# Performance work log

Measured on AMD Instinct MI355X. Metric: run time of the kernel, lower is better.

The kernel has to match this reference:

```python
import jax, jax.numpy as jnp
import numpy as np

N_CENTERS = 100000
N_SPECIES = 4
R_CUT = 5.0
N_MAX_L = [12, 10, 8, 6]  # n_max per angular channel l, from basis_cutoff E_max


def setup_inputs() -> dict:
    key = jax.random.key(0)
    k1, k2, k3, k4 = jax.random.split(key, 4)
    n_pairs = 2000000
    return {
        "direction_vectors": 2.0 * jax.random.normal(k1, (n_pairs, 3), dtype=jnp.float32),
        "pair_center_idx": jax.random.randint(k2, (n_pairs,), 0, N_CENTERS),
        "neighbor_species_idx": jax.random.randint(k3, (n_pairs,), 0, N_SPECIES),
        "center_species_idx": jax.random.randint(k4, (N_CENTERS,), 0, N_SPECIES),
    }


def _radial_basis(r, l, n_max):
    # GTO-style basis with smooth cosine cutoff (stands in for RadialBasis(E_max)).
    r2 = r * r
    fc = jnp.where(r < R_CUT, 0.5 * (jnp.cos(jnp.pi * r / R_CUT) + 1.0), 0.0)
    alphas = (jnp.arange(n_max, dtype=r.dtype) + 1.0) / (R_CUT * R_CUT)
    # [n_pairs, n_max]
    return (r**l * fc)[:, None] * jnp.exp(-alphas[None, :] * r2[:, None])


def reference(direction_vectors, pair_center_idx, neighbor_species_idx, center_species_idx):
    # r = |direction vector| per pair
    r = jnp.sqrt(jnp.sum(direction_vectors * direction_vectors, axis=-1))  # [P]
    # density_indices = center*n_species + species_neighbor (as in index_add_)
    idx = pair_center_idx * N_SPECIES + neighbor_species_idx  # [P]
    feats = []
    for l, n_max in enumerate(N_MAX_L):
        rb = _radial_basis(r, l, n_max)  # [P, n_max]
        dens = jnp.zeros((N_CENTERS * N_SPECIES, n_max), dtype=rb.dtype).at[idx].add(rb)
        # reshape (n_centers, n_species, n) -> swapaxes -> (n_centers, n*n_species)
        dens = dens.reshape(N_CENTERS, N_SPECIES, n_max).swapaxes(1, 2).reshape(N_CENTERS, -1)
        feats.append(dens)
    out = jnp.concatenate(feats, axis=1)  # [n_centers, sum_l n_max_l*n_species]
    # per-species index_select of center rows == stable sort of rows by center species
    order = jnp.argsort(center_species_idx, stable=True)
    return out[order]
```

## Files before the change

### kernel.cpp

```cpp
#include <hip/hip_runtime.h>
#include <hip/hip_bf16.h>

#define NSPEC 4
#define NFEAT 144
#define RCUT 5.0f
#define CPB 256
#define MAXBC 400
#define CAP 5120
#define CHUNK 8192
#define PBDIM 1024
#define IPT (CHUNK / PBDIM)
#define ASTRIDE 148
#define PLDSN (CHUNK + 2 * MAXBC + 16 + 128)


__global__ void zero_f32(float* __restrict__ out, int n) {
    int n4 = n >> 2;
    float4* o4 = (float4*)out;
    for (int i = blockIdx.x * blockDim.x + threadIdx.x; i < n4; i += gridDim.x * blockDim.x)
        o4[i] = make_float4(0.f, 0.f, 0.f, 0.f);
    int tail = n & 3;
    if (blockIdx.x == 0 && threadIdx.x < tail) out[n4 * 4 + threadIdx.x] = 0.f;
}


__global__ void prep_kernel(const int* __restrict__ cs, int n, int* __restrict__ chunkCounts,
                            int* __restrict__ zeroPtr, int zeroN) {
    __shared__ int cnt[NSPEC];
    if (threadIdx.x < NSPEC) cnt[threadIdx.x] = 0;
    __syncthreads();
    int i = blockIdx.x * blockDim.x + threadIdx.x;
    if (i < n) atomicAdd(&cnt[cs[i]], 1);
    if (zeroPtr) {
        for (int j = i; j < zeroN; j += gridDim.x * blockDim.x) zeroPtr[j] = 0;
    }
    __syncthreads();
    if (threadIdx.x < NSPEC) chunkCounts[blockIdx.x * NSPEC + threadIdx.x] = cnt[threadIdx.x];
}


__global__ void __launch_bounds__(PBDIM) partdest_kernel(
        const float* __restrict__ dirs, const int* __restrict__ pci,
        const int* __restrict__ nsi, const int* __restrict__ cs,
        const int* __restrict__ chunkCounts, int* __restrict__ dest,
        int* __restrict__ gCursor, unsigned* __restrict__ gBucket,
        int P, int NC, int nbkc, int nChunks, int nPart) {
    __shared__ int ldsraw[PLDSN];

    int tid = threadIdx.x;
    int lane = tid & 63, wv = tid >> 6;

    if ((int)blockIdx.x < nPart) {
        unsigned* sSort = (unsigned*)ldsraw;
        int* sHist = ldsraw + CHUNK;
        int* sOffs = sHist + MAXBC;
        int* sWaveTot = sOffs + MAXBC;

        int base = blockIdx.x * CHUNK;

        for (int i = tid; i < nbkc; i += PBDIM) sHist[i] = 0;
        __syncthreads();

        unsigned uu[IPT];
        int bb[IPT];
        #pragma unroll
        for (int j = 0; j < IPT; ++j) {
            int i = base + j * PBDIM + tid;
            int bkt = -1; unsigned u = 0;
            if (i < P) {
                float x = dirs[3 * i + 0], y = dirs[3 * i + 1], z = dirs[3 * i + 2];
                float r2 = x * x + y * y + z * z;
                if (r2 < RCUT * RCUT) {
                    float r = sqrtf(r2);
                    int c = pci[i];
                    bkt = c >> 8;
                    u = (__float_as_uint(r) & 0xFFFFFC00u) | ((unsigned)(c & 255) << 2) |
                        (unsigned)nsi[i];
                    atomicAdd(&sHist[bkt], 1);
                }
            }
            uu[j] = u; bb[j] = bkt;
        }
        __syncthreads();

        int run = 0;
        if (tid < nbkc) { sOffs[tid] = 0; run = sHist[tid]; }
        int incl = run;
        #pragma unroll
        for (int off = 1; off < 64; off <<= 1) {
            int t = __shfl_up(incl, off);
            if (lane >= off) incl += t;
        }
        if (lane == 63) sWaveTot[wv] = incl;
        __syncthreads();
        int wbase = 0;
        for (int w = 0; w < wv; ++w) wbase += sWaveTot[w];
        if (tid < nbkc) sOffs[tid] = wbase + incl - run;
        __syncthreads();

        #pragma unroll
        for (int j = 0; j < IPT; ++j) {
            if (bb[j] >= 0) {
                int pos = atomicAdd(&sOffs[bb[j]], 1);
                sSort[pos] = uu[j];
            }
        }
        __syncthreads();

        for (int b = tid; b < nbkc; b += PBDIM) {
            int c = sHist[b];
            if (!c) continue;
            int start = sOffs[b] - c;
            int g = atomicAdd(&gCursor[b], c);
            int lim = min(c, CAP - g);
            unsigned* dst = gBucket + (size_t)b * CAP + g;
            for (int k = 0; k < lim; ++k) dst[k] = sSort[start + k];
        }
    } else {
        int cj = blockIdx.x - nPart;
        if (cj >= nChunks) return;
        int* cOffs = ldsraw;
        int* wPart = ldsraw + 8;
        int* spAcc = ldsraw + 48;
        int* wCnt  = ldsraw + 64;

        int sp = wv & 3;
        int pref = 0, tot = 0;
        for (int c = (wv >> 2) * 64 + lane; c < nChunks; c += 256) {
            int v = chunkCounts[c * NSPEC + sp];
            tot += v;
            if (c < cj) pref += v;
        }
        #pragma unroll
        for (int off = 32; off; off >>= 1) {
            pref += __shfl_down(pref, off);
            tot  += __shfl_down(tot, off);
        }
        if (lane == 0) { wPart[wv * 2] = pref; wPart[wv * 2 + 1] = tot; }
        __syncthreads();

        if (tid < 4) {
            int p = 0, t = 0;
            for (int w = tid; w < 16; w += 4) { p += wPart[w * 2]; t += wPart[w * 2 + 1]; }
            spAcc[tid] = p; spAcc[4 + tid] = t;
        }
        __syncthreads();
        if (tid == 0) {
            int b = 0;
            #pragma unroll
            for (int s = 0; s < NSPEC; ++s) { cOffs[s] = b + spAcc[s]; b += spAcc[4 + s]; }
        }
        __syncthreads();

        int i = cj * 256 + tid;
        int s = (tid < 256 && i < NC) ? cs[i] : -1;
        int lanePrefix = 0;
        #pragma unroll
        for (int spp = 0; spp < NSPEC; ++spp) {
            unsigned long long b = __ballot(s == spp);
            if (lane == 0) wCnt[wv * 4 + spp] = __popcll(b);
            if (spp == s) lanePrefix = __popcll(b & ((1ull << lane) - 1ull));
        }
        __syncthreads();
        if (s >= 0) {
            int wp = 0;
            for (int w = 0; w < wv; ++w) wp += wCnt[w * 4 + s];
            dest[i] = cOffs[s] + wp + lanePrefix;
        }
    }
}


__global__ void __launch_bounds__(PBDIM) accum_kernel(
        const int* __restrict__ gCursor, const unsigned* __restrict__ gBucket,
        const int* __restrict__ dest, float* __restrict__ out, int NC) {
    __shared__ unsigned sSort[CAP];
    __shared__ int sHist[1024];
    __shared__ int sOff[1024];
    __shared__ int sWaveTot[16];
    __shared__ int destLds[CPB];
    __shared__ float sStage[64 * ASTRIDE];

    int tid = threadIdx.x;
    int b = blockIdx.x;
    int cBase = b * CPB;
    int n = min(gCursor[b], CAP);
    const unsigned* src = gBucket + (size_t)b * CAP;

    sHist[tid] = 0;
    if (tid < CPB && cBase + tid < NC) destLds[tid] = dest[cBase + tid];
    __syncthreads();

    for (int i = tid; i < n; i += PBDIM) atomicAdd(&sHist[src[i] & 1023u], 1);
    __syncthreads();

    int lane = tid & 63, wv = tid >> 6;
    int v = sHist[tid];
    int incl = v;
    #pragma unroll
    for (int off = 1; off < 64; off <<= 1) {
        int t = __shfl_up(incl, off);
        if (lane >= off) incl += t;
    }
    if (lane == 63) sWaveTot[wv] = incl;
    __syncthreads();
    int wbase = 0;
    for (int w = 0; w < wv; ++w) wbase += sWaveTot[w];
    sOff[tid] = wbase + incl - v;
    __syncthreads();

    for (int i = tid; i < n; i += PBDIM) {
        unsigned u = src[i];
        int pos = atomicAdd(&sOff[u & 1023u], 1);
        sSort[pos] = u;
    }
    __syncthreads();

    int end = sOff[tid], start = end - sHist[tid];
    float acc[36];
    #pragma unroll
    for (int j = 0; j < 36; ++j) acc[j] = 0.f;

    for (int p = start; p < end; ++p) {
        unsigned u = sSort[p];
        float r = __uint_as_float(u & 0xFFFFFC00u);
        float r2 = r * r;
        float fc = 0.5f * (__cosf(0.6283185307179586f * r) + 1.0f);
        float q = __expf(-r2 * 0.04f);
        float q2 = q * q;
        float bq[12];
        bq[0] = q; bq[1] = q2;
        #pragma unroll
        for (int nn = 2; nn < 12; ++nn) bq[nn] = bq[nn - 2] * q2;
        float a0 = fc, a1 = fc * r, a2 = a1 * r, a3 = a2 * r;
        #pragma unroll
        for (int nn = 0; nn < 12; ++nn) acc[nn]      = fmaf(a0, bq[nn], acc[nn]);
        #pragma unroll
        for (int nn = 0; nn < 10; ++nn) acc[12 + nn] = fmaf(a1, bq[nn], acc[12 + nn]);
        #pragma unroll
        for (int nn = 0; nn < 8; ++nn)  acc[22 + nn] = fmaf(a2, bq[nn], acc[22 + nn]);
        #pragma unroll
        for (int nn = 0; nn < 6; ++nn)  acc[30 + nn] = fmaf(a3, bq[nn], acc[30 + nn]);
    }

    int nRows = min(CPB, NC - cBase);
    #pragma unroll 1
    for (int g = 0; g < 4; ++g) {
        if ((tid >> 8) == g) {
            float* rowp = sStage + ((tid >> 2) & 63) * ASTRIDE + (tid & 3);
            #pragma unroll
            for (int nn = 0; nn < 12; ++nn) rowp[nn * 4]       = acc[nn];
            #pragma unroll
            for (int nn = 0; nn < 10; ++nn) rowp[48 + nn * 4]  = acc[12 + nn];
            #pragma unroll
            for (int nn = 0; nn < 8; ++nn)  rowp[88 + nn * 4]  = acc[22 + nn];
            #pragma unroll
            for (int nn = 0; nn < 6; ++nn)  rowp[120 + nn * 4] = acc[30 + nn];
        }
        __syncthreads();
        int gRows = min(64, nRows - g * 64);
        if (gRows > 0) {
            int lim = gRows * 36;
            for (int i = tid; i < lim; i += PBDIM) {
                int row = i / 36;
                int c4 = i - row * 36;
                float4 val = *(const float4*)(sStage + row * ASTRIDE + c4 * 4);
                *(float4*)(out + (size_t)destLds[g * 64 + row] * NFEAT + c4 * 4) = val;
            }
        }
        __syncthreads();
    }
}


__global__ void pair_kernel(const float* __restrict__ dirs,
                            const int* __restrict__ pci,
                            const int* __restrict__ nsi,
                            const int* __restrict__ dest,
                            float* __restrict__ out, int P) {
    int i = blockIdx.x * blockDim.x + threadIdx.x;
    if (i >= P) return;
    float x = dirs[3 * i + 0], y = dirs[3 * i + 1], z = dirs[3 * i + 2];
    float r2 = x * x + y * y + z * z;
    float r = sqrtf(r2);
    if (r >= RCUT) return;
    float fc = 0.5f * (cosf(3.14159265358979323846f * r * (1.0f / RCUT)) + 1.0f);
    float q = expf(-r2 * (1.0f / (RCUT * RCUT)));
    int rowb = dest[pci[i]] * NFEAT;
    int s = nsi[i];
    float* o = out + rowb + s;
    float rl = fc;
    const int nmax[4] = {12, 10, 8, 6};
    const int offl[4] = {0, 48, 88, 120};
    #pragma unroll
    for (int l = 0; l < 4; ++l) {
        float e = q;
        for (int n = 0; n < nmax[l]; ++n) { atomicAdd(o + offl[l] + n * NSPEC, rl * e); e *= q; }
        rl *= r;
    }
}

extern "C" void kernel_launch(void* const* d_in, const int* in_sizes, int n_in,
                              void* d_out, int out_size, void* d_ws, size_t ws_size,
                              hipStream_t stream) {
    const float* dirs = (const float*)d_in[0];
    const int* pci = (const int*)d_in[1];
    const int* nsi = (const int*)d_in[2];
    const int* cs = (const int*)d_in[3];
    int P = in_sizes[1];
    int NC = in_sizes[3];
    float* out = (float*)d_out;

    int nChunks = (NC + 255) / 256;
    int nbkc = (NC + CPB - 1) / CPB;
    int nPart = (P + CHUNK - 1) / CHUNK;

    int* chunkCounts  = (int*)d_ws;
    int* dest         = chunkCounts + nChunks * NSPEC;
    int* gCursor      = dest + NC;
    unsigned* gBucket = (unsigned*)(gCursor + nbkc);

    size_t need = ((size_t)(nChunks * NSPEC) + (size_t)NC + (size_t)nbkc +
                   (size_t)nbkc * CAP) * sizeof(int);
    bool fastPath = (ws_size >= need) && (nbkc <= MAXBC);

    if (fastPath) {
        prep_kernel<<<nChunks, 256, 0, stream>>>(cs, NC, chunkCounts, gCursor, nbkc);
        partdest_kernel<<<nPart + nChunks, PBDIM, 0, stream>>>(
            dirs, pci, nsi, cs, chunkCounts, dest, gCursor, gBucket,
            P, NC, nbkc, nChunks, nPart);
        accum_kernel<<<nbkc, PBDIM, 0, stream>>>(gCursor, gBucket, dest, out, NC);
    } else {
        prep_kernel<<<nChunks, 256, 0, stream>>>(cs, NC, chunkCounts, (int*)nullptr, 0);
        partdest_kernel<<<nChunks, PBDIM, 0, stream>>>(
            dirs, pci, nsi, cs, chunkCounts, dest, (int*)d_ws , (unsigned*)d_ws,
            0 , NC, nbkc, nChunks, 0);
        zero_f32<<<2048, 256, 0, stream>>>(out, out_size);
        pair_kernel<<<(P + 255) / 256, 256, 0, stream>>>(dirs, pci, nsi, dest, out, P);
    }
}
```

Before: 47.49 us.

## Move per-species destination computation into accum kernel and fold counting into partition

The per-chunk species counting moves into the partition kernel as extra blocks, and the sorted-row destination computation moves into the accumulate kernel, since CPB equals the 256-center chunk size. The global dest array is no longer written and re-read on the fast path, and a tiny kernel now zeroes the bucket cursors. This spreads the small prefix computations across existing launches, but each accumulate block now does the chunk-count prefix scan (up to 391 chunks) before its main work.

```diff
diff --git a/kernel.cpp b/kernel.cpp
--- a/kernel.cpp
+++ b/kernel.cpp
@@ -11,7 +11,7 @@
 #define PBDIM 1024
 #define IPT (CHUNK / PBDIM)
 #define ASTRIDE 148
-#define PLDSN (CHUNK + 2 * MAXBC + 16 + 128)
+#define PLDSN (CHUNK + 2 * MAXBC + 16 + 32)
 
 
 __global__ void zero_f32(float* __restrict__ out, int n) {
@@ -23,26 +23,26 @@
     if (blockIdx.x == 0 && threadIdx.x < tail) out[n4 * 4 + threadIdx.x] = 0.f;
 }
 
-
-__global__ void prep_kernel(const int* __restrict__ cs, int n, int* __restrict__ chunkCounts,
-                            int* __restrict__ zeroPtr, int zeroN) {
+__global__ void zeroCur_kernel(int* __restrict__ p, int n) {
+    for (int i = threadIdx.x; i < n; i += blockDim.x) p[i] = 0;
+}
+
+
+__global__ void prep_kernel(const int* __restrict__ cs, int n, int* __restrict__ chunkCounts) {
     __shared__ int cnt[NSPEC];
     if (threadIdx.x < NSPEC) cnt[threadIdx.x] = 0;
     __syncthreads();
     int i = blockIdx.x * blockDim.x + threadIdx.x;
     if (i < n) atomicAdd(&cnt[cs[i]], 1);
-    if (zeroPtr) {
-        for (int j = i; j < zeroN; j += gridDim.x * blockDim.x) zeroPtr[j] = 0;
-    }
     __syncthreads();
     if (threadIdx.x < NSPEC) chunkCounts[blockIdx.x * NSPEC + threadIdx.x] = cnt[threadIdx.x];
 }
 
 
-__global__ void __launch_bounds__(PBDIM) partdest_kernel(
+__global__ void __launch_bounds__(PBDIM) partprep_kernel(
         const float* __restrict__ dirs, const int* __restrict__ pci,
         const int* __restrict__ nsi, const int* __restrict__ cs,
-        const int* __restrict__ chunkCounts, int* __restrict__ dest,
+        int* __restrict__ chunkCounts,
         int* __restrict__ gCursor, unsigned* __restrict__ gBucket,
         int P, int NC, int nbkc, int nChunks, int nPart) {
     __shared__ int ldsraw[PLDSN];
@@ -84,7 +84,7 @@
         __syncthreads();
 
         int run = 0;
-        if (tid < nbkc) { sOffs[tid] = 0; run = sHist[tid]; }
+        if (tid < nbkc) run = sHist[tid];
         int incl = run;
         #pragma unroll
         for (int off = 1; off < 64; off <<= 1) {
@@ -117,84 +117,93 @@
             for (int k = 0; k < lim; ++k) dst[k] = sSort[start + k];
         }
     } else {
-        int cj = blockIdx.x - nPart;
-        if (cj >= nChunks) return;
-        int* cOffs = ldsraw;
-        int* wPart = ldsraw + 8;
-        int* spAcc = ldsraw + 48;
-        int* wCnt  = ldsraw + 64;
-
-        int sp = wv & 3;
-        int pref = 0, tot = 0;
-        for (int c = (wv >> 2) * 64 + lane; c < nChunks; c += 256) {
-            int v = chunkCounts[c * NSPEC + sp];
-            tot += v;
-            if (c < cj) pref += v;
-        }
-        #pragma unroll
-        for (int off = 32; off; off >>= 1) {
-            pref += __shfl_down(pref, off);
-            tot  += __shfl_down(tot, off);
-        }
-        if (lane == 0) { wPart[wv * 2] = pref; wPart[wv * 2 + 1] = tot; }
-        __syncthreads();
-
-        if (tid < 4) {
-            int p = 0, t = 0;
-            for (int w = tid; w < 16; w += 4) { p += wPart[w * 2]; t += wPart[w * 2 + 1]; }
-            spAcc[tid] = p; spAcc[4 + tid] = t;
-        }
-        __syncthreads();
-        if (tid == 0) {
-            int b = 0;
-            #pragma unroll
-            for (int s = 0; s < NSPEC; ++s) { cOffs[s] = b + spAcc[s]; b += spAcc[4 + s]; }
-        }
-        __syncthreads();
-
-        int i = cj * 256 + tid;
-        int s = (tid < 256 && i < NC) ? cs[i] : -1;
-        int lanePrefix = 0;
-        #pragma unroll
-        for (int spp = 0; spp < NSPEC; ++spp) {
-            unsigned long long b = __ballot(s == spp);
-            if (lane == 0) wCnt[wv * 4 + spp] = __popcll(b);
-            if (spp == s) lanePrefix = __popcll(b & ((1ull << lane) - 1ull));
-        }
-        __syncthreads();
-        if (s >= 0) {
-            int wp = 0;
-            for (int w = 0; w < wv; ++w) wp += wCnt[w * 4 + s];
-            dest[i] = cOffs[s] + wp + lanePrefix;
-        }
+        int grp = tid >> 8;
+        int lt = tid & 255;
+        int* cnt = ldsraw + grp * NSPEC;
+        if (lt < NSPEC) cnt[lt] = 0;
+        __syncthreads();
+        int cj = ((int)blockIdx.x - nPart) * 4 + grp;
+        int i = cj * 256 + lt;
+        if (cj < nChunks && i < NC) atomicAdd(&cnt[cs[i]], 1);
+        __syncthreads();
+        if (cj < nChunks && lt < NSPEC) chunkCounts[cj * NSPEC + lt] = cnt[lt];
     }
 }
 
 
 __global__ void __launch_bounds__(PBDIM) accum_kernel(
         const int* __restrict__ gCursor, const unsigned* __restrict__ gBucket,
-        const int* __restrict__ dest, float* __restrict__ out, int NC) {
+        const int* __restrict__ cs, const int* __restrict__ chunkCounts,
+        float* __restrict__ out, int NC, int nChunks) {
     __shared__ unsigned sSort[CAP];
     __shared__ int sHist[1024];
     __shared__ int sOff[1024];
     __shared__ int sWaveTot[16];
     __shared__ int destLds[CPB];
     __shared__ float sStage[64 * ASTRIDE];
+    __shared__ int wPart[32];
+    __shared__ int spAcc[8];
+    __shared__ int cOffs[4];
+    __shared__ int wCnt[64];
 
     int tid = threadIdx.x;
     int b = blockIdx.x;
     int cBase = b * CPB;
     int n = min(gCursor[b], CAP);
     const unsigned* src = gBucket + (size_t)b * CAP;
+    int lane = tid & 63, wv = tid >> 6;
+
+    {
+        int sp = wv & 3;
+        int pref = 0, tot = 0;
+        for (int c = (wv >> 2) * 64 + lane; c < nChunks; c += 256) {
+            int v = chunkCounts[c * NSPEC + sp];
+            tot += v;
+            if (c < b) pref += v;
+        }
+        #pragma unroll
+        for (int off = 32; off; off >>= 1) {
+            pref += __shfl_down(pref, off);
+            tot  += __shfl_down(tot, off);
+        }
+        if (lane == 0) { wPart[wv * 2] = pref; wPart[wv * 2 + 1] = tot; }
+        __syncthreads();
+        if (tid < 4) {
+            int p = 0, t = 0;
+            for (int w = tid; w < 16; w += 4) { p += wPart[w * 2]; t += wPart[w * 2 + 1]; }
+            spAcc[tid] = p; spAcc[4 + tid] = t;
+        }
+        __syncthreads();
+        if (tid == 0) {
+            int base = 0;
+            #pragma unroll
+            for (int s = 0; s < NSPEC; ++s) { cOffs[s] = base + spAcc[s]; base += spAcc[4 + s]; }
+        }
+        __syncthreads();
+
+        int i = cBase + tid;
+        int s = (tid < 256 && i < NC) ? cs[i] : -1;
+        int lanePrefix = 0;
+        #pragma unroll
+        for (int spp = 0; spp < NSPEC; ++spp) {
+            unsigned long long bl = __ballot(s == spp);
+            if (lane == 0) wCnt[wv * 4 + spp] = __popcll(bl);
+            if (spp == s) lanePrefix = __popcll(bl & ((1ull << lane) - 1ull));
+        }
+        __syncthreads();
+        if (s >= 0) {
+            int wp = 0;
+            for (int w = 0; w < wv; ++w) wp += wCnt[w * 4 + s];
+            destLds[tid] = cOffs[s] + wp + lanePrefix;
+        }
+    }
 
     sHist[tid] = 0;
-    if (tid < CPB && cBase + tid < NC) destLds[tid] = dest[cBase + tid];
     __syncthreads();
 
     for (int i = tid; i < n; i += PBDIM) atomicAdd(&sHist[src[i] & 1023u], 1);
     __syncthreads();
 
-    int lane = tid & 63, wv = tid >> 6;
     int v = sHist[tid];
     int incl = v;
     #pragma unroll
@@ -272,6 +281,61 @@
     }
 }
 
+
+__global__ void __launch_bounds__(PBDIM) dest_kernel(
+        const int* __restrict__ cs, const int* __restrict__ chunkCounts,
+        int* __restrict__ dest, int NC, int nChunks) {
+    __shared__ int cOffs[4];
+    __shared__ int wPart[32];
+    __shared__ int spAcc[8];
+    __shared__ int wCnt[64];
+    int tid = threadIdx.x;
+    int lane = tid & 63, wv = tid >> 6;
+    int cj = blockIdx.x;
+    if (cj >= nChunks) return;
+
+    int sp = wv & 3;
+    int pref = 0, tot = 0;
+    for (int c = (wv >> 2) * 64 + lane; c < nChunks; c += 256) {
+        int v = chunkCounts[c * NSPEC + sp];
+        tot += v;
+        if (c < cj) pref += v;
+    }
+    #pragma unroll
+    for (int off = 32; off; off >>= 1) {
+        pref += __shfl_down(pref, off);
+        tot  += __shfl_down(tot, off);
+    }
+    if (lane == 0) { wPart[wv * 2] = pref; wPart[wv * 2 + 1] = tot; }
+    __syncthreads();
+    if (tid < 4) {
+        int p = 0, t = 0;
+        for (int w = tid; w < 16; w += 4) { p += wPart[w * 2]; t += wPart[w * 2 + 1]; }
+        spAcc[tid] = p; spAcc[4 + tid] = t;
+    }
+    __syncthreads();
+    if (tid == 0) {
+        int b = 0;
+        #pragma unroll
+        for (int s = 0; s < NSPEC; ++s) { cOffs[s] = b + spAcc[s]; b += spAcc[4 + s]; }
+    }
+    __syncthreads();
+    int i = cj * 256 + tid;
+    int s = (tid < 256 && i < NC) ? cs[i] : -1;
+    int lanePrefix = 0;
+    #pragma unroll
+    for (int spp = 0; spp < NSPEC; ++spp) {
+        unsigned long long b = __ballot(s == spp);
+        if (lane == 0) wCnt[wv * 4 + spp] = __popcll(b);
+        if (spp == s) lanePrefix = __popcll(b & ((1ull << lane) - 1ull));
+    }
+    __syncthreads();
+    if (s >= 0) {
+        int wp = 0;
+        for (int w = 0; w < wv; ++w) wp += wCnt[w * 4 + s];
+        dest[i] = cOffs[s] + wp + lanePrefix;
+    }
+}
 
 __global__ void pair_kernel(const float* __restrict__ dirs,
                             const int* __restrict__ pci,
@@ -314,6 +378,7 @@
     int nChunks = (NC + 255) / 256;
     int nbkc = (NC + CPB - 1) / CPB;
     int nPart = (P + CHUNK - 1) / CHUNK;
+    int nPrepB = (nChunks + 3) / 4;
 
     int* chunkCounts  = (int*)d_ws;
     int* dest         = chunkCounts + nChunks * NSPEC;
@@ -322,19 +387,17 @@
 
     size_t need = ((size_t)(nChunks * NSPEC) + (size_t)NC + (size_t)nbkc +
                    (size_t)nbkc * CAP) * sizeof(int);
-    bool fastPath = (ws_size >= need) && (nbkc <= MAXBC);
+    bool fastPath = (ws_size >= need) && (nbkc <= MAXBC) && (CPB == 256);
 
     if (fastPath) {
-        prep_kernel<<<nChunks, 256, 0, stream>>>(cs, NC, chunkCounts, gCursor, nbkc);
-        partdest_kernel<<<nPart + nChunks, PBDIM, 0, stream>>>(
-            dirs, pci, nsi, cs, chunkCounts, dest, gCursor, gBucket,
-            P, NC, nbkc, nChunks, nPart);
-        accum_kernel<<<nbkc, PBDIM, 0, stream>>>(gCursor, gBucket, dest, out, NC);
+        zeroCur_kernel<<<1, 256, 0, stream>>>(gCursor, nbkc);
+        partprep_kernel<<<nPart + nPrepB, PBDIM, 0, stream>>>(
+            dirs, pci, nsi, cs, chunkCounts, gCursor, gBucket, P, NC, nbkc, nChunks, nPart);
+        accum_kernel<<<nbkc, PBDIM, 0, stream>>>(gCursor, gBucket, cs, chunkCounts,
+                                                 out, NC, nChunks);
     } else {
-        prep_kernel<<<nChunks, 256, 0, stream>>>(cs, NC, chunkCounts, (int*)nullptr, 0);
-        partdest_kernel<<<nChunks, PBDIM, 0, stream>>>(
-            dirs, pci, nsi, cs, chunkCounts, dest, (int*)d_ws , (unsigned*)d_ws,
-            0 , NC, nbkc, nChunks, 0);
+        prep_kernel<<<nChunks, 256, 0, stream>>>(cs, NC, chunkCounts);
+        dest_kernel<<<nChunks, PBDIM, 0, stream>>>(cs, chunkCounts, dest, NC, nChunks);
         zero_f32<<<2048, 256, 0, stream>>>(out, out_size);
         pair_kernel<<<(P + 255) / 256, 256, 0, stream>>>(dirs, pci, nsi, dest, out, P);
     }
```

Measured after the change: 49.72 us. 4.7% more time.
